# Performance work log

Hardware: AMD Instinct MI355X
Metric: run time of the kernel (lower is better)

The kernel has to match this reference:

```python
import jax, jax.numpy as jnp
import numpy as np

B, S, D = 4, 2048, 1024   # batch, seq, in_dim
E, K, H = 8, 2, 4096      # num_experts, top_k, expert hidden


def setup_inputs() -> dict:
    key = jax.random.key(0)
    ks = jax.random.split(key, 10)
    s = lambda *sh: 1.0 / np.sqrt(sh[0])
    x = jax.random.normal(ks[0], (B, S, D), dtype=jnp.float32)
    # router: Linear(D,D) + GELU + Linear(D,E), xavier-ish init, zero bias
    Wr1 = jax.random.uniform(ks[1], (D, D), jnp.float32, -s(D), s(D))
    br1 = jnp.zeros((D,), jnp.float32)
    Wr2 = jax.random.uniform(ks[2], (D, E), jnp.float32, -s(D), s(D))
    br2 = jnp.zeros((E,), jnp.float32)
    # experts: stacked 2-layer MLPs, Linear(D,H)+GELU+Linear(H,D)
    W1 = jax.random.uniform(ks[3], (E, D, H), jnp.float32, -s(D), s(D))
    b1 = jnp.zeros((E, H), jnp.float32)
    W2 = jax.random.uniform(ks[4], (E, H, D), jnp.float32, -s(H), s(H))
    b2 = jnp.zeros((E, D), jnp.float32)
    return {"x": x, "Wr1": Wr1, "br1": br1, "Wr2": Wr2, "br2": br2,
            "W1": W1, "b1": b1, "W2": W2, "b2": b2}


def reference(x, Wr1, br1, Wr2, br2, W1, b1, W2, b2):
    T = B * S
    xf = x.reshape(T, D)                                   # [T, D]
    # router MLP -> softmax
    h = jax.nn.gelu(xf @ Wr1 + br1, approximate=False)
    logits = h @ Wr2 + br2                                 # [T, E]
    probs = jax.nn.softmax(logits, axis=-1)
    # top-k selection; scatter selected probs back into a sparse [T, E] map
    top_v, top_i = jax.lax.top_k(probs, K)                 # [T, K]
    rows = jnp.arange(T)[:, None]
    router_probs = jnp.zeros_like(probs).at[rows, top_i].set(top_v)
    # normalize=True, top_k>1: renormalize (gradient flows through sum)
    router_probs = router_probs / router_probs.sum(-1, keepdims=True)
    # combine: sum_e router_probs[:, e] * expert_e(x)
    # (router_probs is exactly zero for non-selected experts, matching the
    #  masked gather/scatter-add in the torch module)
    out = jnp.zeros_like(xf)
    for e in range(E):  # fixed small expert loop
        y = jax.nn.gelu(xf @ W1[e] + b1[e], approximate=False) @ W2[e] + b2[e]
        out = out + router_probs[:, e:e + 1] * y
    return out.reshape(B, S, D)
```

## Files before the change

### kernel.cpp

```cpp
#include <hip/hip_runtime.h>
#include <hip/hip_bf16.h>
#include <math.h>

#define T_TOK 8192
#define DIM   1024
#define NEXP  8
#define TOPK  2
#define HID   4096
#define NSLOT (T_TOK * TOPK)
#define FLAG_GAP 1e-4f
#define MAXFLAG  2048

typedef unsigned short u16;
typedef __bf16 bf16x8 __attribute__((ext_vector_type(8)));
typedef float  f32x4  __attribute__((ext_vector_type(4)));
typedef u16    u16x4  __attribute__((ext_vector_type(4)));

#define GLL16(g, l) \
  __builtin_amdgcn_global_load_lds((__attribute__((address_space(1))) unsigned int*)(g), \
                                   (__attribute__((address_space(3))) unsigned int*)(l), 16, 0, 0)

__device__ __forceinline__ float bf2f(u16 u) {
  union { unsigned int i; float f; } w; w.i = ((unsigned int)u) << 16; return w.f;
}
__device__ __forceinline__ u16 f2bf(float f) {
  union { float f; unsigned int i; } w; w.f = f;
  unsigned int i = w.i;
  return (u16)((i + 0x7FFFu + ((i >> 16) & 1u)) >> 16);
}
__device__ __forceinline__ float gelu_f(float v) {
  return 0.5f * v * (1.0f + erff(v * 0.70710678118654752f));
}

__global__ __launch_bounds__(256) void split_cast(
    const float* __restrict__ in, u16* __restrict__ hi, u16* __restrict__ lo, int n4)
{
  int i = blockIdx.x * 256 + threadIdx.x;
  if (i >= n4) return;
  f32x4 v = *(const f32x4*)&in[(size_t)i * 4];
  u16x4 h, l;
#pragma unroll
  for (int j = 0; j < 4; j++) {
    h[j] = f2bf(v[j]);
    l[j] = f2bf(v[j] - bf2f(h[j]));
  }
  *(u16x4*)&hi[(size_t)i * 4] = h;
  *(u16x4*)&lo[(size_t)i * 4] = l;
}

__global__ __launch_bounds__(256) void transpose_cast(
    const float* __restrict__ in, u16* __restrict__ out, int R, int C)
{
  __shared__ u16 ld[64][65];
  const size_t mat = (size_t)R * C;
  const float* I = in + (size_t)blockIdx.z * mat;
  u16* O = out + (size_t)blockIdx.z * mat;
  const int c0 = blockIdx.x * 64, r0 = blockIdx.y * 64;
  const int tx = threadIdx.x & 15, ty = threadIdx.x >> 4;
#pragma unroll
  for (int p = 0; p < 4; p++) {
    int r = ty + p * 16;
    f32x4 v = *(const f32x4*)&I[(size_t)(r0 + r) * C + c0 + tx * 4];
    ld[r][tx * 4 + 0] = f2bf(v.x); ld[r][tx * 4 + 1] = f2bf(v.y);
    ld[r][tx * 4 + 2] = f2bf(v.z); ld[r][tx * 4 + 3] = f2bf(v.w);
  }
  __syncthreads();
#pragma unroll
  for (int p = 0; p < 4; p++) {
    int c = ty + p * 16;
    u16x4 v;
    v.x = ld[tx * 4 + 0][c]; v.y = ld[tx * 4 + 1][c];
    v.z = ld[tx * 4 + 2][c]; v.w = ld[tx * 4 + 3][c];
    *(u16x4*)&O[(size_t)(c0 + c) * R + r0 + tx * 4] = v;
  }
}

__global__ __launch_bounds__(256) void transpose_cast_split(
    const float* __restrict__ in, u16* __restrict__ Ohi, u16* __restrict__ Olo,
    int R, int C)
{
  __shared__ float ld[64][65];
  const int c0 = blockIdx.x * 64, r0 = blockIdx.y * 64;
  const int tx = threadIdx.x & 15, ty = threadIdx.x >> 4;
#pragma unroll
  for (int p = 0; p < 4; p++) {
    int r = ty + p * 16;
    f32x4 v = *(const f32x4*)&in[(size_t)(r0 + r) * C + c0 + tx * 4];
    ld[r][tx * 4 + 0] = v.x; ld[r][tx * 4 + 1] = v.y;
    ld[r][tx * 4 + 2] = v.z; ld[r][tx * 4 + 3] = v.w;
  }
  __syncthreads();
#pragma unroll
  for (int p = 0; p < 4; p++) {
    int c = ty + p * 16;
    u16x4 h, l;
#pragma unroll
    for (int j = 0; j < 4; j++) {
      float v = ld[tx * 4 + j][c];
      h[j] = f2bf(v);
      l[j] = f2bf(v - bf2f(h[j]));
    }
    *(u16x4*)&Ohi[(size_t)(c0 + c) * R + r0 + tx * 4] = h;
    *(u16x4*)&Olo[(size_t)(c0 + c) * R + r0 + tx * 4] = l;
  }
}

__global__ __launch_bounds__(256) void gemm1_split(
    const u16* __restrict__ Ahi, const u16* __restrict__ Alo,
    const u16* __restrict__ Bhi, const u16* __restrict__ Blo,
    const float* __restrict__ bias, float* __restrict__ Cout)
{
  const int r0 = blockIdx.y * 128, n0 = blockIdx.x * 128;
  __shared__ __align__(16) u16 Ah[128 * 32], Al[128 * 32];
  __shared__ __align__(16) u16 Bh[128 * 32], Bl[128 * 32];

  const int tid = threadIdx.x;
  const int wave = tid >> 6, lane = tid & 63;
  const int srow = lane >> 2, scol = (lane & 3) * 8;

  const u16 *aph[2], *apl[2], *bph[2], *bpl[2];
  u16 *ahd[2], *ald[2], *bhd[2], *bld[2];
#pragma unroll
  for (int i = 0; i < 2; i++) {
    int r = wave * 32 + i * 16 + srow;
    size_t arow = (size_t)(r0 + r) * DIM + scol;
    size_t brow = (size_t)(n0 + r) * DIM + scol;
    aph[i] = Ahi + arow; apl[i] = Alo + arow;
    bph[i] = Bhi + brow; bpl[i] = Blo + brow;
    ahd[i] = &Ah[(wave * 32 + i * 16) * 32]; ald[i] = &Al[(wave * 32 + i * 16) * 32];
    bhd[i] = &Bh[(wave * 32 + i * 16) * 32]; bld[i] = &Bl[(wave * 32 + i * 16) * 32];
  }

  f32x4 zero = {0.f, 0.f, 0.f, 0.f};
  f32x4 acc[4][4];
#pragma unroll
  for (int a = 0; a < 4; a++)
#pragma unroll
    for (int b = 0; b < 4; b++) acc[a][b] = zero;

  const int quad = lane >> 4, l16 = lane & 15;
  const int wm = (wave & 1) * 64, wn = (wave >> 1) * 64;

  for (int k0 = 0; k0 < DIM; k0 += 32) {
#pragma unroll
    for (int i = 0; i < 2; i++) {
      GLL16(aph[i] + k0, ahd[i]);
      GLL16(apl[i] + k0, ald[i]);
      GLL16(bph[i] + k0, bhd[i]);
      GLL16(bpl[i] + k0, bld[i]);
    }
    __syncthreads();
    bf16x8 ah[4], al[4], bh[4], bl[4];
#pragma unroll
    for (int mt = 0; mt < 4; mt++) {
      int ro = (wm + mt * 16 + l16) * 32 + quad * 8;
      ah[mt] = *(const bf16x8*)&Ah[ro];
      al[mt] = *(const bf16x8*)&Al[ro];
    }
#pragma unroll
    for (int nt = 0; nt < 4; nt++) {
      int ro = (wn + nt * 16 + l16) * 32 + quad * 8;
      bh[nt] = *(const bf16x8*)&Bh[ro];
      bl[nt] = *(const bf16x8*)&Bl[ro];
    }
#pragma unroll
    for (int mt = 0; mt < 4; mt++)
#pragma unroll
      for (int nt = 0; nt < 4; nt++) {
        acc[mt][nt] = __builtin_amdgcn_mfma_f32_16x16x32_bf16(ah[mt], bh[nt], acc[mt][nt], 0, 0, 0);
        acc[mt][nt] = __builtin_amdgcn_mfma_f32_16x16x32_bf16(ah[mt], bl[nt], acc[mt][nt], 0, 0, 0);
        acc[mt][nt] = __builtin_amdgcn_mfma_f32_16x16x32_bf16(al[mt], bh[nt], acc[mt][nt], 0, 0, 0);
      }
    __syncthreads();
  }

  float bv[4];
#pragma unroll
  for (int nt = 0; nt < 4; nt++) bv[nt] = bias[n0 + wn + nt * 16 + l16];

#pragma unroll
  for (int mt = 0; mt < 4; mt++)
#pragma unroll
    for (int reg = 0; reg < 4; reg++) {
      int r = wm + mt * 16 + quad * 4 + reg;
      size_t crow = (size_t)(r0 + r) * DIM;
#pragma unroll
      for (int nt = 0; nt < 4; nt++) {
        int c = n0 + wn + nt * 16 + l16;
        Cout[crow + c] = gelu_f(acc[mt][nt][reg] + bv[nt]);
      }
    }
}

template<int EPI, bool GATHER>
__global__ __launch_bounds__(256) void gemm_bt(
    const u16* __restrict__ A, const u16* __restrict__ BT,
    const float* __restrict__ bias,
    const int* __restrict__ counts, const int* __restrict__ offs,
    const int* __restrict__ tok,
    void* __restrict__ Cout, int M, int N, int K)
{
  const int e   = blockIdx.z;
  const int cnt = counts ? counts[e] : M;
  const int r0  = blockIdx.y * 128;
  if (r0 >= cnt) return;
  const int base = offs ? offs[e] : 0;
  const int n0   = blockIdx.x * 128;
  const u16* BTe = BT + (size_t)e * N * K;
  const float* be = bias + (size_t)e * N;

  __shared__ __align__(16) u16 As[128 * 32];
  __shared__ __align__(16) u16 Bs[128 * 32];

  const int tid = threadIdx.x;
  const int wave = tid >> 6, lane = tid & 63;
  const int srow = lane >> 2, scol = (lane & 3) * 8;

  const u16* ap[2]; const u16* bp[2];
  u16* asd[2]; u16* bsd[2];
#pragma unroll
  for (int i = 0; i < 2; i++) {
    int r  = wave * 32 + i * 16 + srow;
    int rr = min(r0 + r, cnt - 1);
    int arow = GATHER ? tok[base + rr] : (base + rr);
    ap[i] = A + (size_t)arow * K + scol;
    int nr = n0 + wave * 32 + i * 16 + srow;
    bp[i] = BTe + (size_t)nr * K + scol;
    asd[i] = &As[(wave * 32 + i * 16) * 32];
    bsd[i] = &Bs[(wave * 32 + i * 16) * 32];
  }

  f32x4 zero = {0.f, 0.f, 0.f, 0.f};
  f32x4 acc[4][4];
#pragma unroll
  for (int a = 0; a < 4; a++)
#pragma unroll
    for (int b = 0; b < 4; b++) acc[a][b] = zero;

  const int quad = lane >> 4, l16 = lane & 15;
  const int wm = (wave & 1) * 64, wn = (wave >> 1) * 64;

  for (int k0 = 0; k0 < K; k0 += 32) {
#pragma unroll
    for (int i = 0; i < 2; i++) {
      GLL16(ap[i] + k0, asd[i]);
      GLL16(bp[i] + k0, bsd[i]);
    }
    __syncthreads();
    bf16x8 af[4], bfv[4];
#pragma unroll
    for (int mt = 0; mt < 4; mt++)
      af[mt] = *(const bf16x8*)&As[(wm + mt * 16 + l16) * 32 + quad * 8];
#pragma unroll
    for (int nt = 0; nt < 4; nt++)
      bfv[nt] = *(const bf16x8*)&Bs[(wn + nt * 16 + l16) * 32 + quad * 8];
#pragma unroll
    for (int mt = 0; mt < 4; mt++)
#pragma unroll
      for (int nt = 0; nt < 4; nt++)
        acc[mt][nt] = __builtin_amdgcn_mfma_f32_16x16x32_bf16(
            af[mt], bfv[nt], acc[mt][nt], 0, 0, 0);
    __syncthreads();
  }

  float bv[4];
#pragma unroll
  for (int nt = 0; nt < 4; nt++) bv[nt] = be[n0 + wn + nt * 16 + l16];

#pragma unroll
  for (int mt = 0; mt < 4; mt++)
#pragma unroll
    for (int reg = 0; reg < 4; reg++) {
      int r = wm + mt * 16 + quad * 4 + reg;
      if (r0 + r < cnt) {
        size_t crow = (size_t)(base + r0 + r) * N;
#pragma unroll
        for (int nt = 0; nt < 4; nt++) {
          int c = n0 + wn + nt * 16 + l16;
          float v = acc[mt][nt][reg] + bv[nt];
          if (EPI == 0) ((u16*)Cout)[crow + c] = f2bf(gelu_f(v));
          else          ((float*)Cout)[crow + c] = v;
        }
      }
    }
}

__global__ __launch_bounds__(256) void router2a(
    const float* __restrict__ hr, const float* __restrict__ Wr2,
    const float* __restrict__ br2,
    float* __restrict__ logits, int* __restrict__ nflag, int* __restrict__ flaglist)
{
  __shared__ float w[NEXP * DIM];
  __shared__ float bsh[NEXP];
  const int tid = threadIdx.x;
  for (int i = tid; i < NEXP * DIM; i += 256) {
    int d = i >> 3, e2 = i & 7;
    w[e2 * DIM + d] = Wr2[i];
  }
  if (tid < NEXP) bsh[tid] = br2[tid];
  __syncthreads();
  const int wave = tid >> 6, lane = tid & 63;
  for (int tt = 0; tt < 4; tt++) {
    int t = blockIdx.x * 16 + wave * 4 + tt;
    float acc[NEXP] = {0, 0, 0, 0, 0, 0, 0, 0};
    for (int jj = 0; jj < 16; jj++) {
      int d = jj * 64 + lane;
      float hv = hr[(size_t)t * DIM + d];
#pragma unroll
      for (int e2 = 0; e2 < NEXP; e2++) acc[e2] += hv * w[e2 * DIM + d];
    }
#pragma unroll
    for (int off = 32; off > 0; off >>= 1)
#pragma unroll
      for (int e2 = 0; e2 < NEXP; e2++) acc[e2] += __shfl_xor(acc[e2], off, 64);
    if (lane == 0) {
      float l[NEXP];
#pragma unroll
      for (int e2 = 0; e2 < NEXP; e2++) {
        l[e2] = acc[e2] + bsh[e2];
        logits[(size_t)t * NEXP + e2] = l[e2];
      }
      int e0 = 0;
#pragma unroll
      for (int e2 = 1; e2 < NEXP; e2++) if (l[e2] > l[e0]) e0 = e2;
      int e1 = (e0 == 0) ? 1 : 0;
#pragma unroll
      for (int e2 = 0; e2 < NEXP; e2++) if (e2 != e0 && l[e2] > l[e1]) e1 = e2;
      float third = -1e30f;
#pragma unroll
      for (int e2 = 0; e2 < NEXP; e2++)
        if (e2 != e0 && e2 != e1 && l[e2] > third) third = l[e2];
      if (l[e1] - third < FLAG_GAP) {
        int idx = atomicAdd(nflag, 1);
        if (idx < MAXFLAG) flaglist[idx] = t;
      }
    }
  }
}

__global__ __launch_bounds__(256) void fixup_fp64(
    const float* __restrict__ x, const float* __restrict__ Wr1,
    const float* __restrict__ br1, const float* __restrict__ Wr2,
    const float* __restrict__ br2,
    const int* __restrict__ nflag, const int* __restrict__ flaglist,
    float* __restrict__ logits)
{
  int nf = *nflag; if (nf > MAXFLAG) nf = MAXFLAG;
  if ((int)blockIdx.x >= nf) return;
  const int t = flaglist[blockIdx.x];
  __shared__ float xs[DIM];
  __shared__ double part[256][NEXP];
  const int tid = threadIdx.x;
  for (int i = tid; i < DIM; i += 256) xs[i] = x[(size_t)t * DIM + i];
  __syncthreads();
  double h[4] = {0.0, 0.0, 0.0, 0.0};
  const int d0 = tid * 4;
  for (int k = 0; k < DIM; k++) {
    double xv = (double)xs[k];
    f32x4 wv = *(const f32x4*)&Wr1[(size_t)k * DIM + d0];
#pragma unroll
    for (int j = 0; j < 4; j++) h[j] = fma(xv, (double)wv[j], h[j]);
  }
  double lacc[NEXP] = {0, 0, 0, 0, 0, 0, 0, 0};
#pragma unroll
  for (int j = 0; j < 4; j++) {
    double v = h[j] + (double)br1[d0 + j];
    v = 0.5 * v * (1.0 + erf(v * 0.70710678118654752440));
#pragma unroll
    for (int e2 = 0; e2 < NEXP; e2++)
      lacc[e2] = fma(v, (double)Wr2[(size_t)(d0 + j) * NEXP + e2], lacc[e2]);
  }
#pragma unroll
  for (int e2 = 0; e2 < NEXP; e2++) part[tid][e2] = lacc[e2];
  __syncthreads();
  if (tid < NEXP) {
    double s = (double)br2[tid];
    for (int i = 0; i < 256; i++) s += part[i][tid];
    logits[(size_t)t * NEXP + tid] = (float)s;
  }
}

__global__ __launch_bounds__(256) void finalize_route(
    const float* __restrict__ logits, float2* __restrict__ gates,
    int* __restrict__ experts, int* __restrict__ counts)
{
  __shared__ int lc[NEXP];
  const int tid = threadIdx.x;
  if (tid < NEXP) lc[tid] = 0;
  __syncthreads();
  const int t = blockIdx.x * 256 + tid;
  float l[NEXP];
#pragma unroll
  for (int e2 = 0; e2 < NEXP; e2++) l[e2] = logits[(size_t)t * NEXP + e2];
  int e0 = 0;
#pragma unroll
  for (int e2 = 1; e2 < NEXP; e2++) if (l[e2] > l[e0]) e0 = e2;
  int e1 = (e0 == 0) ? 1 : 0;
#pragma unroll
  for (int e2 = 0; e2 < NEXP; e2++) if (e2 != e0 && l[e2] > l[e1]) e1 = e2;
  float p1 = expf(l[e1] - l[e0]);
  float s = 1.0f + p1;
  gates[t] = make_float2(1.0f / s, p1 / s);
  experts[2 * t]     = e0;
  experts[2 * t + 1] = e1;
  atomicAdd(&lc[e0], 1); atomicAdd(&lc[e1], 1);
  __syncthreads();
  if (tid < NEXP && lc[tid]) atomicAdd(&counts[tid], lc[tid]);
}

__global__ void zero_meta(int* meta) {
  if (threadIdx.x < 32) meta[threadIdx.x] = 0;
}

__global__ void prefix8(const int* __restrict__ counts, int* __restrict__ offs,
                        int* __restrict__ cursor) {
  if (threadIdx.x == 0) {
    int a = 0;
    for (int e = 0; e < NEXP; e++) { offs[e] = a; cursor[e] = a; a += counts[e]; }
  }
}

__global__ __launch_bounds__(256) void scatter_tok(
    const int* __restrict__ experts, int* __restrict__ cursor,
    int* __restrict__ tok_of_slot, int* __restrict__ slot_of_token)
{
  int idx = blockIdx.x * 256 + threadIdx.x;
  int e = experts[idx];
  int slot = atomicAdd(&cursor[e], 1);
  tok_of_slot[slot] = idx >> 1;
  slot_of_token[idx] = slot;
}

__global__ __launch_bounds__(256) void combine(
    const float* __restrict__ y, const float2* __restrict__ gates,
    const int* __restrict__ slot_of_token, float* __restrict__ out)
{
  int t = blockIdx.x, tid = threadIdx.x;
  int s0 = slot_of_token[2 * t], s1 = slot_of_token[2 * t + 1];
  float2 g = gates[t];
  f32x4 a = *(const f32x4*)&y[(size_t)s0 * DIM + tid * 4];
  f32x4 b = *(const f32x4*)&y[(size_t)s1 * DIM + tid * 4];
  f32x4 o;
#pragma unroll
  for (int j = 0; j < 4; j++) o[j] = g.x * a[j] + g.y * b[j];
  *(f32x4*)&out[(size_t)t * DIM + tid * 4] = o;
}

extern "C" void kernel_launch(void* const* d_in, const int* in_sizes, int n_in,
                              void* d_out, int out_size, void* d_ws, size_t ws_size,
                              hipStream_t stream)
{
  const float* x   = (const float*)d_in[0];
  const float* Wr1 = (const float*)d_in[1];
  const float* br1 = (const float*)d_in[2];
  const float* Wr2 = (const float*)d_in[3];
  const float* br2 = (const float*)d_in[4];
  const float* W1  = (const float*)d_in[5];
  const float* b1  = (const float*)d_in[6];
  const float* W2  = (const float*)d_in[7];
  const float* b2  = (const float*)d_in[8];
  float* out = (float*)d_out;

  char* ws = (char*)d_ws;
  const size_t MB = 1024 * 1024;
  u16*   xhi    = (u16*)  (ws + 0 * MB);
  u16*   xlo    = (u16*)  (ws + 16 * MB);
  u16*   Wr1Thi = (u16*)  (ws + 32 * MB);
  u16*   Wr1Tlo = (u16*)  (ws + 34 * MB);
  u16*   W1T    = (u16*)  (ws + 36 * MB);
  u16*   W2T    = (u16*)  (ws + 100 * MB);
  u16*   hidden = (u16*)  (ws + 164 * MB);
  float* hr32   = (float*)(ws + 164 * MB);
  float* y      = (float*)(ws + 0 * MB);
  char* tail = ws + 292 * MB;
  float*  logits = (float*)tail;                      tail += (size_t)T_TOK * NEXP * 4;
  float2* gates  = (float2*)tail;                     tail += (size_t)T_TOK * 8;
  int* experts       = (int*)tail;                    tail += (size_t)NSLOT * 4;
  int* tok_of_slot   = (int*)tail;                    tail += (size_t)NSLOT * 4;
  int* slot_of_token = (int*)tail;                    tail += (size_t)NSLOT * 4;
  int* flaglist      = (int*)tail;                    tail += (size_t)MAXFLAG * 4;
  int* meta          = (int*)tail;
  int* counts = meta, *offs = meta + 8, *cursor = meta + 16, *nflag = meta + 24;

  zero_meta<<<1, 64, 0, stream>>>(meta);
  split_cast<<<T_TOK * DIM / 1024, 256, 0, stream>>>(x, xhi, xlo, T_TOK * DIM / 4);
  transpose_cast_split<<<dim3(16, 16, 1), 256, 0, stream>>>(Wr1, Wr1Thi, Wr1Tlo, DIM, DIM);
  transpose_cast<<<dim3(64, 16, NEXP), 256, 0, stream>>>(W1, W1T, DIM, HID);
  transpose_cast<<<dim3(16, 64, NEXP), 256, 0, stream>>>(W2, W2T, HID, DIM);
  gemm1_split<<<dim3(DIM / 128, T_TOK / 128), 256, 0, stream>>>(
      xhi, xlo, Wr1Thi, Wr1Tlo, br1, hr32);
  router2a<<<T_TOK / 16, 256, 0, stream>>>(hr32, Wr2, br2, logits, nflag, flaglist);
  fixup_fp64<<<MAXFLAG, 256, 0, stream>>>(x, Wr1, br1, Wr2, br2, nflag, flaglist, logits);
  finalize_route<<<T_TOK / 256, 256, 0, stream>>>(logits, gates, experts, counts);
  prefix8<<<1, 64, 0, stream>>>(counts, offs, cursor);
  scatter_tok<<<NSLOT / 256, 256, 0, stream>>>(experts, cursor,
                                               tok_of_slot, slot_of_token);
  gemm_bt<0, true><<<dim3(HID / 128, NSLOT / 128, NEXP), 256, 0, stream>>>(
      xhi, W1T, b1, counts, offs, tok_of_slot, hidden, NSLOT, HID, DIM);
  gemm_bt<1, false><<<dim3(DIM / 128, NSLOT / 128, NEXP), 256, 0, stream>>>(
      hidden, W2T, b2, counts, offs, nullptr, y, NSLOT, DIM, HID);
  combine<<<T_TOK, 256, 0, stream>>>(y, gates, slot_of_token, out);
}
```

Baseline: 1.136 ms.

## Compact expert GEMM grid via block map and store expert outputs as bf16

Prefix kernel now builds a compact list of (expert, row-block) pairs, so the two expert GEMMs launch MBLK row-blocks instead of NSLOT/128 × NEXP blocks, most of which previously exited early. The second GEMM writes its output in bf16 instead of fp32, halving y traffic, and combine converts back to float. This removes launch and scheduling cost for empty blocks and cuts memory traffic, at the cost of extra bf16 rounding of expert outputs and a fixed upper bound of 136 row-blocks.

```diff
diff --git a/kernel.cpp b/kernel.cpp
--- a/kernel.cpp
+++ b/kernel.cpp
@@ -10,6 +10,7 @@
 #define NSLOT (T_TOK * TOPK)
 #define FLAG_GAP 1e-4f
 #define MAXFLAG  2048
+#define MBLK     136
 
 typedef unsigned short u16;
 typedef __bf16 bf16x8 __attribute__((ext_vector_type(8)));
@@ -197,14 +198,16 @@
     const u16* __restrict__ A, const u16* __restrict__ BT,
     const float* __restrict__ bias,
     const int* __restrict__ counts, const int* __restrict__ offs,
+    const int* __restrict__ map_e, const int* __restrict__ map_r0,
     const int* __restrict__ tok,
-    void* __restrict__ Cout, int M, int N, int K)
-{
-  const int e   = blockIdx.z;
-  const int cnt = counts ? counts[e] : M;
-  const int r0  = blockIdx.y * 128;
-  if (r0 >= cnt) return;
-  const int base = offs ? offs[e] : 0;
+    u16* __restrict__ Cout, int N, int K)
+{
+  const int mb = blockIdx.y;
+  const int e  = map_e[mb];
+  if (e < 0) return;
+  const int cnt  = counts[e];
+  const int r0   = map_r0[mb];
+  const int base = offs[e];
   const int n0   = blockIdx.x * 128;
   const u16* BTe = BT + (size_t)e * N * K;
   const float* be = bias + (size_t)e * N;
@@ -278,8 +281,7 @@
         for (int nt = 0; nt < 4; nt++) {
           int c = n0 + wn + nt * 16 + l16;
           float v = acc[mt][nt][reg] + bv[nt];
-          if (EPI == 0) ((u16*)Cout)[crow + c] = f2bf(gelu_f(v));
-          else          ((float*)Cout)[crow + c] = v;
+          Cout[crow + c] = f2bf(EPI == 0 ? gelu_f(v) : v);
         }
       }
     }
@@ -413,10 +415,17 @@
 }
 
 __global__ void prefix8(const int* __restrict__ counts, int* __restrict__ offs,
-                        int* __restrict__ cursor) {
+                        int* __restrict__ cursor,
+                        int* __restrict__ map_e, int* __restrict__ map_r0) {
   if (threadIdx.x == 0) {
-    int a = 0;
-    for (int e = 0; e < NEXP; e++) { offs[e] = a; cursor[e] = a; a += counts[e]; }
+    int a = 0, m = 0;
+    for (int e = 0; e < NEXP; e++) {
+      offs[e] = a; cursor[e] = a;
+      int nb = (counts[e] + 127) >> 7;
+      for (int j = 0; j < nb; j++) { map_e[m] = e; map_r0[m] = j << 7; m++; }
+      a += counts[e];
+    }
+    for (; m < MBLK; m++) { map_e[m] = -1; map_r0[m] = 0; }
   }
 }
 
@@ -432,17 +441,17 @@
 }
 
 __global__ __launch_bounds__(256) void combine(
-    const float* __restrict__ y, const float2* __restrict__ gates,
+    const u16* __restrict__ y, const float2* __restrict__ gates,
     const int* __restrict__ slot_of_token, float* __restrict__ out)
 {
   int t = blockIdx.x, tid = threadIdx.x;
   int s0 = slot_of_token[2 * t], s1 = slot_of_token[2 * t + 1];
   float2 g = gates[t];
-  f32x4 a = *(const f32x4*)&y[(size_t)s0 * DIM + tid * 4];
-  f32x4 b = *(const f32x4*)&y[(size_t)s1 * DIM + tid * 4];
+  u16x4 a = *(const u16x4*)&y[(size_t)s0 * DIM + tid * 4];
+  u16x4 b = *(const u16x4*)&y[(size_t)s1 * DIM + tid * 4];
   f32x4 o;
 #pragma unroll
-  for (int j = 0; j < 4; j++) o[j] = g.x * a[j] + g.y * b[j];
+  for (int j = 0; j < 4; j++) o[j] = g.x * bf2f(a[j]) + g.y * bf2f(b[j]);
   *(f32x4*)&out[(size_t)t * DIM + tid * 4] = o;
 }
 
@@ -471,7 +480,7 @@
   u16*   W2T    = (u16*)  (ws + 100 * MB);
   u16*   hidden = (u16*)  (ws + 164 * MB);
   float* hr32   = (float*)(ws + 164 * MB);
-  float* y      = (float*)(ws + 0 * MB);
+  u16*   y      = (u16*)  (ws + 0 * MB);
   char* tail = ws + 292 * MB;
   float*  logits = (float*)tail;                      tail += (size_t)T_TOK * NEXP * 4;
   float2* gates  = (float2*)tail;                     tail += (size_t)T_TOK * 8;
@@ -479,6 +488,8 @@
   int* tok_of_slot   = (int*)tail;                    tail += (size_t)NSLOT * 4;
   int* slot_of_token = (int*)tail;                    tail += (size_t)NSLOT * 4;
   int* flaglist      = (int*)tail;                    tail += (size_t)MAXFLAG * 4;
+  int* map_e         = (int*)tail;                    tail += (size_t)MBLK * 4;
+  int* map_r0        = (int*)tail;                    tail += (size_t)MBLK * 4;
   int* meta          = (int*)tail;
   int* counts = meta, *offs = meta + 8, *cursor = meta + 16, *nflag = meta + 24;
 
@@ -492,12 +503,12 @@
   router2a<<<T_TOK / 16, 256, 0, stream>>>(hr32, Wr2, br2, logits, nflag, flaglist);
   fixup_fp64<<<MAXFLAG, 256, 0, stream>>>(x, Wr1, br1, Wr2, br2, nflag, flaglist, logits);
   finalize_route<<<T_TOK / 256, 256, 0, stream>>>(logits, gates, experts, counts);
-  prefix8<<<1, 64, 0, stream>>>(counts, offs, cursor);
+  prefix8<<<1, 64, 0, stream>>>(counts, offs, cursor, map_e, map_r0);
   scatter_tok<<<NSLOT / 256, 256, 0, stream>>>(experts, cursor,
                                                tok_of_slot, slot_of_token);
-  gemm_bt<0, true><<<dim3(HID / 128, NSLOT / 128, NEXP), 256, 0, stream>>>(
-      xhi, W1T, b1, counts, offs, tok_of_slot, hidden, NSLOT, HID, DIM);
-  gemm_bt<1, false><<<dim3(DIM / 128, NSLOT / 128, NEXP), 256, 0, stream>>>(
-      hidden, W2T, b2, counts, offs, nullptr, y, NSLOT, DIM, HID);
+  gemm_bt<0, true><<<dim3(HID / 128, MBLK), 256, 0, stream>>>(
+      xhi, W1T, b1, counts, offs, map_e, map_r0, tok_of_slot, hidden, HID, DIM);
+  gemm_bt<1, false><<<dim3(DIM / 128, MBLK), 256, 0, stream>>>(
+      hidden, W2T, b2, counts, offs, map_e, map_r0, nullptr, y, DIM, HID);
   combine<<<T_TOK, 256, 0, stream>>>(y, gates, slot_of_token, out);
 }
```

Result: slower. 1.190 ms (+4.8%).
